# Optimization experiments

Hardware: AMD Instinct MI355X
Metric: run time of the kernel (lower is better)

The kernel has to match this reference:

```python
import jax, jax.numpy as jnp
import numpy as np

B, F, H, OUT, S = 32768, 256, 128, 64, 6
RELAX, EPS, BN_EPS = 1.5, 1e-05, 1e-05
SQRT_HALF = 0.7071067811865476


def _bn(h, g, b):
    # training-mode BatchNorm1d: biased batch statistics over dim 0
    m = h.mean(axis=0)
    v = h.var(axis=0)
    return (h - m) * jax.lax.rsqrt(v + BN_EPS) * g + b


def _tfrm(x, W, g, b, glu_act=True):
    h = _bn(x @ W, g, b)
    if glu_act:
        d = h.shape[1] // 2
        h = h[:, :d] * jax.nn.sigmoid(h[:, d:])
    return h


def setup_inputs() -> dict:
    key = jax.random.key(0)
    ks = jax.random.split(key, 6)
    f32 = jnp.float32
    return {
        "x": jax.random.normal(ks[0], (B, F), f32),
        "enc_g": jnp.ones((F,), f32), "enc_b": jnp.zeros((F,), f32),
        "W1": jax.random.normal(ks[1], (F, 2 * H), f32) * 0.05,
        "g1": jnp.ones((2 * H,), f32), "b1": jnp.zeros((2 * H,), f32),
        "W2": jax.random.normal(ks[2], (H, 2 * H), f32) * 0.05,
        "g2": jnp.ones((2 * H,), f32), "b2": jnp.zeros((2 * H,), f32),
        "W3": jax.random.normal(ks[3], (S, H, 2 * H), f32) * 0.05,
        "g3": jnp.ones((S, 2 * H), f32), "b3": jnp.zeros((S, 2 * H), f32),
        "W4": jax.random.normal(ks[4], (S, H, 2 * H), f32) * 0.05,
        "g4": jnp.ones((S, 2 * H), f32), "b4": jnp.zeros((S, 2 * H), f32),
        "Wc": jax.random.normal(ks[5], (S - 1, OUT, F), f32) * 0.05,
        "gc": jnp.ones((S - 1, F), f32), "bc": jnp.zeros((S - 1, F), f32),
    }


def reference(x, enc_g, enc_b, W1, g1, b1, W2, g2, b2, W3, g3, b3,
              W4, g4, b4, Wc, gc, bc):
    x = _bn(x, enc_g, enc_b)                      # [B, F]
    masked = x
    compl = jnp.ones((x.shape[0], F), x.dtype)    # complementary aggregated mask
    agg_out, agg_entropy = [], []
    for ni in range(S):
        h = _tfrm(masked, W1, g1, b1)                             # [B, H]
        h = (_tfrm(h, W2, g2, b2) + h) * SQRT_HALF
        h = (_tfrm(h, W3[ni], g3[ni], b3[ni]) + h) * SQRT_HALF
        h = (_tfrm(h, W4[ni], g4[ni], b4[ni]) + h) * SQRT_HALF
        if ni > 0:
            # NOTE: source uses x (not h) here -- replicated faithfully
            agg_out.append(jax.nn.relu(x[:, :OUT]))
        fc = h[:, OUT:]                                           # [B, OUT]
        if ni < S - 1:
            coef = _tfrm(fc, Wc[ni], gc[ni], bc[ni], glu_act=False)  # [B, F]
            mask_values = jax.nn.softmax(coef * compl, axis=1)
            compl = compl * (RELAX - mask_values)
            agg_entropy.append(
                jnp.mean(jnp.sum(-mask_values * jnp.log(mask_values + EPS), axis=1))
                / (S - 1))
            masked = mask_values * x
    out = jnp.sum(jnp.stack(agg_out, axis=0), axis=0)   # [B, OUT]
    entropy = jnp.sum(jnp.stack(agg_entropy))           # scalar
    return (out, entropy)
```

## Files before the change

kernel.cpp:

```cpp
#include <hip/hip_runtime.h>
#include <math.h>

#define BSZ   32768
#define FDIM  256
#define HDIM  128
#define OUTD  64
#define SQRT_HALF 0.70710678118654752f
#define BN_EPS 1e-5f
#define SM_EPS 1e-5f
#define INV_B (1.0f / 32768.0f)
#define NCPY  8
#define SLOT  (NCPY * 512)
#define GRID  1024

#define SWZ(r, cb) ((((r) << 9) + (cb)) ^ (((r) & 7) << 4))

typedef __attribute__((ext_vector_type(8))) short bf16x8;
typedef __attribute__((ext_vector_type(4))) short bf16x4;
typedef __attribute__((ext_vector_type(4))) float f32x4;

__device__ __forceinline__ float b2f(unsigned short u) {
    return __uint_as_float(((unsigned int)u) << 16);
}
__device__ __forceinline__ unsigned short f2b(float f) {
    unsigned int u = __float_as_uint(f);
    u += 0x7fff + ((u >> 16) & 1);
    return (unsigned short)(u >> 16);
}

__device__ __forceinline__ void async16(const void* g, void* l) {
    __builtin_amdgcn_global_load_lds(
        (const __attribute__((address_space(1))) void*)(uintptr_t)g,
        (__attribute__((address_space(3))) void*)(unsigned int)(uintptr_t)l,
        16, 0, 0);
}

__device__ inline float waveMaxAll(float v) {
#pragma unroll
    for (int m = 32; m > 0; m >>= 1) v = fmaxf(v, __shfl_xor(v, m, 64));
    return v;
}
__device__ inline float waveSumAll(float v) {
#pragma unroll
    for (int m = 32; m > 0; m >>= 1) v += __shfl_xor(v, m, 64);
    return v;
}

__device__ __forceinline__ void grid_sync_tree(unsigned int* arr, unsigned int want,
                                               int bid, int tid) {
    __syncthreads();
    if (tid == 0) {
        __threadfence();
        __hip_atomic_fetch_add(&arr[(bid & 63) << 5], 1u,
                               __ATOMIC_RELEASE, __HIP_MEMORY_SCOPE_AGENT);
    }
    if (tid < 64) {
        unsigned int* p = &arr[tid << 5];
        long spin = 0;
        while (__hip_atomic_load(p, __ATOMIC_ACQUIRE, __HIP_MEMORY_SCOPE_AGENT) < want) {
            if (++spin > (1L << 24)) break;
            __builtin_amdgcn_s_sleep(1);
        }
        __threadfence();
    }
    __syncthreads();
}

__device__ __forceinline__ void stage_B(short* Bs, const unsigned short* __restrict__ Wt,
                                        int K, int k0, int wave, int lane) {
    const int sr = lane >> 2;
    const int sc = (lane & 3) * 8;
#pragma unroll
    for (int t = 0; t < 4; ++t) {
        const int wr = wave * 64 + t * 16 + sr;
        async16(Wt + (size_t)wr * K + k0 + sc, (void*)(Bs + (wave * 4 + t) * 512 + lane * 8));
    }
}

__device__ __forceinline__ void gemm_core(const short* buf, short* Bs,
                                          const unsigned short* __restrict__ Wt, int K,
                                          int wave, int lane, f32x4 (&acc)[2][4]) {
    const int fm = lane & 15;
    const int fq = (lane >> 4) * 8;
#pragma unroll
    for (int i = 0; i < 2; ++i)
#pragma unroll
        for (int j = 0; j < 4; ++j)
            acc[i][j] = (f32x4){0.f, 0.f, 0.f, 0.f};

    for (int k0 = 0; k0 < K; k0 += 32) {
        __syncthreads();
        bf16x8 af[2], bfr[4];
#pragma unroll
        for (int i = 0; i < 2; ++i)
            af[i] = *(const bf16x8*)((const char*)buf + SWZ(i * 16 + fm, (k0 + fq) * 2));
#pragma unroll
        for (int j = 0; j < 4; ++j)
            bfr[j] = *(const bf16x8*)(Bs + (wave * 64 + j * 16 + fm) * 32 + fq);
#pragma unroll
        for (int i = 0; i < 2; ++i)
#pragma unroll
            for (int j = 0; j < 4; ++j)
                acc[i][j] = __builtin_amdgcn_mfma_f32_16x16x32_bf16(af[i], bfr[j], acc[i][j], 0, 0, 0);
        __syncthreads();
        if (k0 + 32 < K) stage_B(Bs, Wt, K, k0 + 32, wave, lane);
    }
}

__device__ __forceinline__ void stage_epilogue(f32x4 (&acc)[2][4], short* buf,
                                               float* redS, float* redQ,
                                               float* __restrict__ statsOut,
                                               int wave, int lane, int tid, int bcp) {
    const int fm = lane & 15;
    const int row4 = (lane >> 4) * 4;
    const int ocol = wave * 64 + fm;
#pragma unroll
    for (int i = 0; i < 2; ++i)
#pragma unroll
        for (int j = 0; j < 4; ++j)
#pragma unroll
            for (int r = 0; r < 4; ++r)
                *(short*)((char*)buf + SWZ(row4 + i * 16 + r, (ocol + j * 16) * 2)) =
                    (short)f2b(acc[i][j][r]);

#pragma unroll
    for (int j = 0; j < 4; ++j) {
        float s = 0.f, q = 0.f;
#pragma unroll
        for (int i = 0; i < 2; ++i)
#pragma unroll
            for (int r = 0; r < 4; ++r) {
                float v = acc[i][j][r];
                s += v; q += v * v;
            }
        s += __shfl_xor(s, 16, 64); s += __shfl_xor(s, 32, 64);
        q += __shfl_xor(q, 16, 64); q += __shfl_xor(q, 32, 64);
        if (lane < 16) {
            redS[wave * 64 + j * 16 + lane] = s;
            redQ[wave * 64 + j * 16 + lane] = q;
        }
    }
    __syncthreads();
    atomicAdd(&statsOut[bcp + tid], redS[tid]);
    atomicAdd(&statsOut[bcp + 256 + tid], redQ[tid]);
}

__device__ __forceinline__ void build_tbl_glu(const float* __restrict__ st,
                                              const float* __restrict__ pg,
                                              const float* __restrict__ pb,
                                              int colOff, int K, int tid, float* tbl) {
    if (tid < K) {
        const int ch = colOff + tid;
        const int cg = ch + 128;
        float sA = 0.f, qA = 0.f, sG = 0.f, qG = 0.f;
#pragma unroll
        for (int cp = 0; cp < NCPY; ++cp) {
            const float* p = st + cp * 512;
            sA += p[ch]; qA += p[256 + ch];
            sG += p[cg]; qG += p[256 + cg];
        }
        float ma = sA * INV_B, va = qA * INV_B - ma * ma;
        float scA = pg[ch] * rsqrtf(va + BN_EPS);
        tbl[tid] = scA; tbl[K + tid] = pb[ch] - ma * scA;
        float mg = sG * INV_B, vg = qG * INV_B - mg * mg;
        float scG = pg[cg] * rsqrtf(vg + BN_EPS);
        tbl[2 * K + tid] = scG; tbl[3 * K + tid] = pb[cg] - mg * scG;
    }
    __syncthreads();
}

__device__ __forceinline__ void build_tbl_mask(const float* __restrict__ st,
                                               const float* __restrict__ gcp,
                                               const float* __restrict__ bcp_,
                                               int tid, float* tbl) {
    float s = 0.f, q = 0.f;
#pragma unroll
    for (int cp = 0; cp < NCPY; ++cp) {
        s += st[cp * 512 + tid];
        q += st[cp * 512 + 256 + tid];
    }
    float mean = s * INV_B, var = q * INV_B - mean * mean;
    float scl = gcp[tid] * rsqrtf(var + BN_EPS);
    tbl[tid] = scl;
    tbl[256 + tid] = bcp_[tid] - mean * scl;
    __syncthreads();
}

template <int K, bool RES, bool WH, int RB>
__device__ __forceinline__ void glu_prologue(short* buf, const float* tbl,
                                             int tid, int colOff, bf16x4* h) {
    const int ar = tid >> 3;
    const int ac = (tid & 7) * 4;
#pragma unroll
    for (int c = 0; c < K / 32; ++c) {
        const int kk = c * 32 + ac;
        bf16x4 lo = *(const bf16x4*)((const char*)buf + SWZ(ar, (colOff + kk) * 2));
        bf16x4 hi = *(const bf16x4*)((const char*)buf + SWZ(ar, (colOff + kk + 128) * 2));
        float4 a0 = *(const float4*)&tbl[kk];
        float4 h0 = *(const float4*)&tbl[K + kk];
        float4 g0 = *(const float4*)&tbl[2 * K + kk];
        float4 s0 = *(const float4*)&tbl[3 * K + kk];
        const float scA[4] = {a0.x, a0.y, a0.z, a0.w};
        const float shA[4] = {h0.x, h0.y, h0.z, h0.w};
        const float scG[4] = {g0.x, g0.y, g0.z, g0.w};
        const float shG[4] = {s0.x, s0.y, s0.z, s0.w};
        bf16x4 o4;
#pragma unroll
        for (int e = 0; e < 4; ++e) {
            float na = b2f((unsigned short)lo[e]) * scA[e] + shA[e];
            float ng = b2f((unsigned short)hi[e]) * scG[e] + shG[e];
            float v = na * (1.0f / (1.0f + __expf(-ng)));
            if (RES) v = (v + b2f((unsigned short)h[RB + c][e])) * SQRT_HALF;
            o4[e] = (short)f2b(v);
        }
        *(bf16x4*)((char*)buf + SWZ(ar, kk * 2)) = o4;
        if (WH) h[c] = o4;
    }
}

template <int MODE>
__device__ __forceinline__ void mask_phase(short* buf, const float* tbl,
                                           const unsigned short* __restrict__ xb,
                                           unsigned short* cmpl, float* ent, float* went,
                                           int tid, int wave, int lane, int row0, int bid) {
    const int r = tid >> 3;
    const int cq = tid & 7;
    const size_t grow = (size_t)(row0 + r) * 256;

    float l[32];
    float mx = -1e30f;
#pragma unroll
    for (int e = 0; e < 4; ++e) {
        const int c = cq * 32 + e * 8;
        bf16x8 pv = *(const bf16x8*)((const char*)buf + SWZ(r, c * 2));
        bf16x8 cv;
        if (MODE != 0) cv = *(const bf16x8*)(cmpl + grow + c);
        float4 s0 = *(const float4*)&tbl[c], s1 = *(const float4*)&tbl[c + 4];
        float4 h0 = *(const float4*)&tbl[256 + c], h1 = *(const float4*)&tbl[256 + c + 4];
        const float* sp0 = (const float*)&s0; const float* sp1 = (const float*)&s1;
        const float* hp0 = (const float*)&h0; const float* hp1 = (const float*)&h1;
#pragma unroll
        for (int t = 0; t < 8; ++t) {
            float scl = (t < 4) ? sp0[t] : sp1[t - 4];
            float shf = (t < 4) ? hp0[t] : hp1[t - 4];
            float cl = (MODE != 0) ? b2f((unsigned short)cv[t]) : 1.0f;
            float v = (b2f((unsigned short)pv[t]) * scl + shf) * cl;
            l[e * 8 + t] = v;
            mx = fmaxf(mx, v);
        }
    }
    mx = fmaxf(mx, __shfl_xor(mx, 1, 64));
    mx = fmaxf(mx, __shfl_xor(mx, 2, 64));
    mx = fmaxf(mx, __shfl_xor(mx, 4, 64));

    float ssum = 0.f;
#pragma unroll
    for (int i = 0; i < 32; ++i) { l[i] = __expf(l[i] - mx); ssum += l[i]; }
    ssum += __shfl_xor(ssum, 1, 64);
    ssum += __shfl_xor(ssum, 2, 64);
    ssum += __shfl_xor(ssum, 4, 64);
    const float inv = 1.0f / ssum;

    float et = 0.f;
#pragma unroll
    for (int e = 0; e < 4; ++e) {
        const int c = cq * 32 + e * 8;
        bf16x8 xv, cv2;
        if (MODE != 2) xv = *(const bf16x8*)(xb + grow + c);
        if (MODE == 1) cv2 = *(const bf16x8*)(cmpl + grow + c);
        bf16x8 mo, co;
#pragma unroll
        for (int t = 0; t < 8; ++t) {
            float m = l[e * 8 + t] * inv;
            et -= m * __logf(m + SM_EPS);
            if (MODE != 2) {
                float cl = (MODE == 1) ? b2f((unsigned short)cv2[t]) : 1.0f;
                co[t] = (short)f2b(cl * (1.5f - m));
                mo[t] = (short)f2b(m * b2f((unsigned short)xv[t]));
            }
        }
        if (MODE != 2) {
            *(bf16x8*)(cmpl + grow + c) = co;
            *(bf16x8*)((char*)buf + SWZ(r, c * 2)) = mo;
        }
    }
    et += __shfl_xor(et, 1, 64);
    et += __shfl_xor(et, 2, 64);
    et += __shfl_xor(et, 4, 64);
    float wet = waveSumAll(et) * 0.125f;
    if (lane == 0) went[wave] = wet;
    __syncthreads();
    if (tid == 0) {
        float v = went[0] + went[1] + went[2] + went[3];
        atomicAdd(&ent[(bid & 255) << 5], v * (INV_B * 0.2f));
    }
}

__global__ __launch_bounds__(256, 4) void mega(
    const float* __restrict__ x,
    const float* __restrict__ enc_g, const float* __restrict__ enc_b,
    const float* __restrict__ g1, const float* __restrict__ b1,
    const float* __restrict__ g2, const float* __restrict__ b2,
    const float* __restrict__ g3, const float* __restrict__ b3,
    const float* __restrict__ g4, const float* __restrict__ b4,
    const float* __restrict__ gc, const float* __restrict__ bc,
    const float* __restrict__ W1f, const float* __restrict__ W2f,
    const float* __restrict__ W3f, const float* __restrict__ W4f,
    const float* __restrict__ Wcf,
    unsigned short* __restrict__ W1t, unsigned short* __restrict__ W2t,
    unsigned short* __restrict__ W3t, unsigned short* __restrict__ W4t,
    unsigned short* __restrict__ Wct,
    unsigned short* __restrict__ xb, unsigned short* __restrict__ cmpl,
    float* __restrict__ stats, float* __restrict__ ent,
    unsigned int* __restrict__ bar,
    float* __restrict__ out)
{
    __shared__ short buf[32 * 256];
    __shared__ short Bs[256 * 32];
    __shared__ float redS[256], redQ[256];
    __shared__ float tbl[512];
    __shared__ float went[4];

    const int tid  = threadIdx.x;
    const int wave = tid >> 6;
    const int lane = tid & 63;
    const int bid  = blockIdx.x;
    const int row0 = bid * 32;
    const int bcp  = (bid & (NCPY - 1)) * 512;

    unsigned int bgen = 0;
#define GSYNC() do { ++bgen; grid_sync_tree(bar, bgen * 16u, bid, tid); } while (0)

    if (bid < 136) {
        const int m = bid >> 3, kz = bid & 7, n = tid;
        const float* src; unsigned short* dst; int K;
        if (m == 0)      { src = W1f;                        dst = W1t;               K = 256; }
        else if (m == 1) { src = W2f;                        dst = W2t;               K = 128; }
        else if (m < 7)  { int i = m - 2;  src = W3f + (size_t)i * 128 * 256; dst = W3t + (size_t)i * 32768; K = 128; }
        else if (m < 12) { int i = m - 7;  src = W4f + (size_t)i * 128 * 256; dst = W4t + (size_t)i * 32768; K = 128; }
        else             { int i = m - 12; src = Wcf + (size_t)i * 64 * 256;  dst = Wct + (size_t)i * 16384; K = 64; }
        const int k0 = kz * 32;
        if (k0 < K)
            for (int k = k0; k < k0 + 32; ++k)
                dst[(size_t)n * K + k] = f2b(src[(size_t)k * 256 + n]);
    }
    {
        float* red = (float*)buf;
        const int sub = wave;
        const int c4  = lane << 2;
        float s[4] = {0.f, 0.f, 0.f, 0.f}, q[4] = {0.f, 0.f, 0.f, 0.f};
#pragma unroll 8
        for (int i = 0; i < 8; ++i) {
            const int row = row0 + i * 4 + sub;
            float4 v = *(const float4*)(x + (size_t)row * 256 + c4);
            s[0] += v.x; q[0] += v.x * v.x;
            s[1] += v.y; q[1] += v.y * v.y;
            s[2] += v.z; q[2] += v.z * v.z;
            s[3] += v.w; q[3] += v.w * v.w;
        }
#pragma unroll
        for (int e = 0; e < 4; ++e) {
            red[sub * 512 + c4 + e] = s[e];
            red[sub * 512 + 256 + c4 + e] = q[e];
        }
        __syncthreads();
        float sS = red[tid] + red[512 + tid] + red[1024 + tid] + red[1536 + tid];
        float sQ = red[256 + tid] + red[768 + tid] + red[1280 + tid] + red[1792 + tid];
        atomicAdd(&stats[bcp + tid], sS);
        atomicAdd(&stats[bcp + 256 + tid], sQ);
    }
    GSYNC();

    stage_B(Bs, W1t, 256, 0, wave, lane);
    {
        float s = 0.f, q = 0.f;
#pragma unroll
        for (int cp = 0; cp < NCPY; ++cp) {
            s += stats[cp * 512 + tid];
            q += stats[cp * 512 + 256 + tid];
        }
        float mean = s * INV_B, var = q * INV_B - mean * mean;
        float scl = enc_g[tid] * rsqrtf(var + BN_EPS);
        tbl[tid] = scl;
        tbl[256 + tid] = enc_b[tid] - mean * scl;
    }
    __syncthreads();
    {
        const int r = tid >> 3, cq = tid & 7;
        const size_t grow = (size_t)(row0 + r) * 256;
#pragma unroll
        for (int e = 0; e < 4; ++e) {
            const int c = cq * 32 + e * 8;
            float4 xa = *(const float4*)(x + grow + c);
            float4 xc = *(const float4*)(x + grow + c + 4);
            const float xv[8] = {xa.x, xa.y, xa.z, xa.w, xc.x, xc.y, xc.z, xc.w};
            float4 s0 = *(const float4*)&tbl[c], s1 = *(const float4*)&tbl[c + 4];
            float4 f0 = *(const float4*)&tbl[256 + c], f1 = *(const float4*)&tbl[256 + c + 4];
            const float sc[8] = {s0.x, s0.y, s0.z, s0.w, s1.x, s1.y, s1.z, s1.w};
            const float sh[8] = {f0.x, f0.y, f0.z, f0.w, f1.x, f1.y, f1.z, f1.w};
            float n[8];
            bf16x8 o8;
#pragma unroll
            for (int t = 0; t < 8; ++t) {
                n[t] = xv[t] * sc[t] + sh[t];
                o8[t] = (short)f2b(n[t]);
            }
            *(bf16x8*)((char*)buf + SWZ(r, c * 2)) = o8;
            *(bf16x8*)(xb + grow + c) = o8;
            if (c < OUTD) {
                float4 o1 = make_float4(5.f * fmaxf(n[0], 0.f), 5.f * fmaxf(n[1], 0.f),
                                        5.f * fmaxf(n[2], 0.f), 5.f * fmaxf(n[3], 0.f));
                float4 o2 = make_float4(5.f * fmaxf(n[4], 0.f), 5.f * fmaxf(n[5], 0.f),
                                        5.f * fmaxf(n[6], 0.f), 5.f * fmaxf(n[7], 0.f));
                *(float4*)(out + (size_t)(row0 + r) * OUTD + c) = o1;
                *(float4*)(out + (size_t)(row0 + r) * OUTD + c + 4) = o2;
            }
        }
    }

    f32x4 acc[2][4];
    bf16x4 h[4];

    for (int ni = 0; ni < 5; ++ni) {
        float* s1 = stats + (size_t)(1 + ni * 5 + 0) * SLOT;
        float* s2 = stats + (size_t)(1 + ni * 5 + 1) * SLOT;
        float* s3 = stats + (size_t)(1 + ni * 5 + 2) * SLOT;
        float* s4 = stats + (size_t)(1 + ni * 5 + 3) * SLOT;
        float* s5 = stats + (size_t)(1 + ni * 5 + 4) * SLOT;

        if (ni > 0) {
            float* s5p = stats + (size_t)(1 + (ni - 1) * 5 + 4) * SLOT;
            build_tbl_mask(s5p, gc + (ni - 1) * 256, bc + (ni - 1) * 256, tid, tbl);
            if (ni == 1)
                mask_phase<0>(buf, tbl, xb, cmpl, ent, went, tid, wave, lane, row0, bid);
            else
                mask_phase<1>(buf, tbl, xb, cmpl, ent, went, tid, wave, lane, row0, bid);
        }
        gemm_core(buf, Bs, W1t, 256, wave, lane, acc);
        stage_epilogue(acc, buf, redS, redQ, s1, wave, lane, tid, bcp);
        stage_B(Bs, W2t, 128, 0, wave, lane);
        GSYNC();

        build_tbl_glu(s1, g1, b1, 0, 128, tid, tbl);
        glu_prologue<128, false, true, 0>(buf, tbl, tid, 0, h);
        gemm_core(buf, Bs, W2t, 128, wave, lane, acc);
        stage_epilogue(acc, buf, redS, redQ, s2, wave, lane, tid, bcp);
        stage_B(Bs, W3t + (size_t)ni * 32768, 128, 0, wave, lane);
        GSYNC();

        build_tbl_glu(s2, g2, b2, 0, 128, tid, tbl);
        glu_prologue<128, true, true, 0>(buf, tbl, tid, 0, h);
        gemm_core(buf, Bs, W3t + (size_t)ni * 32768, 128, wave, lane, acc);
        stage_epilogue(acc, buf, redS, redQ, s3, wave, lane, tid, bcp);
        stage_B(Bs, W4t + (size_t)ni * 32768, 128, 0, wave, lane);
        GSYNC();

        build_tbl_glu(s3, g3 + ni * 256, b3 + ni * 256, 0, 128, tid, tbl);
        glu_prologue<128, true, true, 0>(buf, tbl, tid, 0, h);
        gemm_core(buf, Bs, W4t + (size_t)ni * 32768, 128, wave, lane, acc);
        stage_epilogue(acc, buf, redS, redQ, s4, wave, lane, tid, bcp);
        stage_B(Bs, Wct + (size_t)ni * 16384, 64, 0, wave, lane);
        GSYNC();

        build_tbl_glu(s4, g4 + ni * 256, b4 + ni * 256, 64, 64, tid, tbl);
        glu_prologue<64, true, false, 2>(buf, tbl, tid, 64, h);
        gemm_core(buf, Bs, Wct + (size_t)ni * 16384, 64, wave, lane, acc);
        stage_epilogue(acc, buf, redS, redQ, s5, wave, lane, tid, bcp);
        if (ni < 4) stage_B(Bs, W1t, 256, 0, wave, lane);
        GSYNC();
    }

    build_tbl_mask(stats + (size_t)(1 + 4 * 5 + 4) * SLOT,
                   gc + 4 * 256, bc + 4 * 256, tid, tbl);
    mask_phase<2>(buf, tbl, xb, cmpl, ent, went, tid, wave, lane, row0, bid);
    GSYNC();

    if (bid == 0 && wave == 0) {
        float v = 0.f;
#pragma unroll
        for (int i = 0; i < 4; ++i) v += ent[(lane + 64 * i) << 5];
        v = waveSumAll(v);
        if (lane == 0) out[(size_t)BSZ * OUTD] = v;
    }
#undef GSYNC
}

__global__ __launch_bounds__(256) void prep_w(
    const float* __restrict__ W1, const float* __restrict__ W2,
    const float* __restrict__ W3, const float* __restrict__ W4,
    const float* __restrict__ Wc,
    unsigned short* __restrict__ W1t, unsigned short* __restrict__ W2t,
    unsigned short* __restrict__ W3t, unsigned short* __restrict__ W4t,
    unsigned short* __restrict__ Wct)
{
    const int m = blockIdx.x, kz = blockIdx.y, n = threadIdx.x;
    const float* src; unsigned short* dst; int K;
    if (m == 0)      { src = W1;                        dst = W1t;               K = 256; }
    else if (m == 1) { src = W2;                        dst = W2t;               K = 128; }
    else if (m < 7)  { int i = m - 2;  src = W3 + (size_t)i * 128 * 256; dst = W3t + (size_t)i * 32768; K = 128; }
    else if (m < 12) { int i = m - 7;  src = W4 + (size_t)i * 128 * 256; dst = W4t + (size_t)i * 32768; K = 128; }
    else             { int i = m - 12; src = Wc + (size_t)i * 64 * 256;  dst = Wct + (size_t)i * 16384; K = 64; }
    const int k0 = kz * 32;
    if (k0 >= K) return;
    for (int k = k0; k < k0 + 32; ++k)
        dst[(size_t)n * K + k] = f2b(src[(size_t)k * 256 + n]);
}

__global__ __launch_bounds__(256) void colstats(const float* __restrict__ X,
                                                float* __restrict__ st0) {
    __shared__ float red[4][512];
    const int sub = threadIdx.x >> 6;
    const int c4  = (threadIdx.x & 63) << 2;
    float s[4] = {0.f, 0.f, 0.f, 0.f}, q[4] = {0.f, 0.f, 0.f, 0.f};
#pragma unroll 8
    for (int i = 0; i < 8; ++i) {
        const int row = blockIdx.x * 32 + i * 4 + sub;
        float4 v = *(const float4*)(X + (size_t)row * 256 + c4);
        s[0] += v.x; q[0] += v.x * v.x;
        s[1] += v.y; q[1] += v.y * v.y;
        s[2] += v.z; q[2] += v.z * v.z;
        s[3] += v.w; q[3] += v.w * v.w;
    }
#pragma unroll
    for (int e = 0; e < 4; ++e) {
        red[sub][c4 + e] = s[e];
        red[sub][256 + c4 + e] = q[e];
    }
    __syncthreads();
    const int t = threadIdx.x;
    const int cp = (blockIdx.x & (NCPY - 1)) * 512;
    float sS = red[0][t] + red[1][t] + red[2][t] + red[3][t];
    float sQ = red[0][256 + t] + red[1][256 + t] + red[2][256 + t] + red[3][256 + t];
    atomicAdd(&st0[cp + t], sS);
    atomicAdd(&st0[cp + 256 + t], sQ);
}

__global__ __launch_bounds__(256) void norm_x(const float* __restrict__ x,
                                              const float* __restrict__ st0,
                                              const float* __restrict__ g,
                                              const float* __restrict__ b,
                                              unsigned short* __restrict__ xb,
                                              float* __restrict__ out) {
    const int i4 = blockIdx.x * 256 + threadIdx.x;
    const int row = i4 >> 6, c4 = (i4 & 63) << 2;
    float4 xv = *(const float4*)(x + (size_t)row * 256 + c4);
    float sS[4] = {0.f, 0.f, 0.f, 0.f}, sQ[4] = {0.f, 0.f, 0.f, 0.f};
#pragma unroll
    for (int cp = 0; cp < NCPY; ++cp) {
        float4 a = *(const float4*)&st0[cp * 512 + c4];
        float4 q = *(const float4*)&st0[cp * 512 + 256 + c4];
        sS[0] += a.x; sS[1] += a.y; sS[2] += a.z; sS[3] += a.w;
        sQ[0] += q.x; sQ[1] += q.y; sQ[2] += q.z; sQ[3] += q.w;
    }
    float4 gv = *(const float4*)&g[c4];
    float4 bv = *(const float4*)&b[c4];
    const float* xp = (const float*)&xv;
    const float* gp = (const float*)&gv; const float* bp = (const float*)&bv;
    float n[4];
    ushort4 ob;
    unsigned short* obp = (unsigned short*)&ob;
#pragma unroll
    for (int e = 0; e < 4; ++e) {
        float mean = sS[e] * INV_B;
        float var  = sQ[e] * INV_B - mean * mean;
        float sc   = gp[e] * rsqrtf(var + BN_EPS);
        float sh   = bp[e] - mean * sc;
        n[e] = xp[e] * sc + sh;
        obp[e] = f2b(n[e]);
    }
    *(ushort4*)(xb + (size_t)row * 256 + c4) = ob;
    if (c4 < OUTD) {
        float4 ov = make_float4(5.0f * fmaxf(n[0], 0.f), 5.0f * fmaxf(n[1], 0.f),
                                5.0f * fmaxf(n[2], 0.f), 5.0f * fmaxf(n[3], 0.f));
        *(float4*)(out + (size_t)row * OUTD + c4) = ov;
    }
}

__device__ __forceinline__ void gemm_epilogue(
    f32x4 (&acc)[2][4], int row0, int wave, int lane, int tid, int bcp,
    float* redS, float* redQ,
    unsigned short* __restrict__ Pout, float* __restrict__ statsOut)
{
    const int fm = lane & 15;
    const int orow = row0 + (lane >> 4) * 4;
    const int ocol = wave * 64 + fm;
#pragma unroll
    for (int i = 0; i < 2; ++i)
#pragma unroll
        for (int j = 0; j < 4; ++j)
#pragma unroll
            for (int r = 0; r < 4; ++r)
                Pout[(size_t)(orow + i * 16 + r) * 256 + (ocol + j * 16)] = f2b(acc[i][j][r]);

#pragma unroll
    for (int j = 0; j < 4; ++j) {
        float s = 0.f, q = 0.f;
#pragma unroll
        for (int i = 0; i < 2; ++i)
#pragma unroll
            for (int r = 0; r < 4; ++r) {
                float v = acc[i][j][r];
                s += v; q += v * v;
            }
        s += __shfl_xor(s, 16, 64); s += __shfl_xor(s, 32, 64);
        q += __shfl_xor(q, 16, 64); q += __shfl_xor(q, 32, 64);
        if (lane < 16) {
            redS[wave * 64 + j * 16 + lane] = s;
            redQ[wave * 64 + j * 16 + lane] = q;
        }
    }
    __syncthreads();
    atomicAdd(&statsOut[bcp + tid], redS[tid]);
    atomicAdd(&statsOut[bcp + 256 + tid], redQ[tid]);
}

__global__ __launch_bounds__(256) void gemm_bf16(
    const unsigned short* __restrict__ A,
    const unsigned short* __restrict__ Wt, int K,
    unsigned short* __restrict__ P,
    float* __restrict__ statsOut)
{
    __shared__ short As[32 * 32];
    __shared__ short Bs[256 * 32];
    __shared__ float redS[256], redQ[256];

    const int tid  = threadIdx.x;
    const int wave = tid >> 6;
    const int lane = tid & 63;
    const int row0 = blockIdx.x * 32;
    const int bcp  = (blockIdx.x & (NCPY - 1)) * 512;

    const int sr = lane >> 2;
    const int sc = (lane & 3) * 8;
    const int fm = lane & 15;
    const int fq = (lane >> 4) * 8;

    f32x4 acc[2][4];
#pragma unroll
    for (int i = 0; i < 2; ++i)
#pragma unroll
        for (int j = 0; j < 4; ++j)
            acc[i][j] = (f32x4){0.f, 0.f, 0.f, 0.f};

    for (int k0 = 0; k0 < K; k0 += 32) {
        if (wave < 2)
            async16(A + (size_t)(row0 + wave * 16 + sr) * K + k0 + sc,
                    (void*)(As + wave * 512 + lane * 8));
#pragma unroll
        for (int t = 0; t < 4; ++t) {
            const int wr = wave * 64 + t * 16 + sr;
            async16(Wt + (size_t)wr * K + k0 + sc,
                    (void*)(Bs + (wave * 4 + t) * 512 + lane * 8));
        }
        __syncthreads();

        bf16x8 af[2], bfr[4];
#pragma unroll
        for (int i = 0; i < 2; ++i)
            af[i] = *(const bf16x8*)(As + (i * 16 + fm) * 32 + fq);
#pragma unroll
        for (int j = 0; j < 4; ++j)
            bfr[j] = *(const bf16x8*)(Bs + (wave * 64 + j * 16 + fm) * 32 + fq);
#pragma unroll
        for (int i = 0; i < 2; ++i)
#pragma unroll
            for (int j = 0; j < 4; ++j)
                acc[i][j] = __builtin_amdgcn_mfma_f32_16x16x32_bf16(af[i], bfr[j], acc[i][j], 0, 0, 0);
        __syncthreads();
    }

    gemm_epilogue(acc, row0, wave, lane, tid, bcp, redS, redQ, P, statsOut);
}

template <int MODE>
__global__ __launch_bounds__(256) void gemm_mask(
    const unsigned short* Pc,
    const float* __restrict__ cstats,
    const float* __restrict__ gc, const float* __restrict__ bc,
    const unsigned short* __restrict__ xb,
    unsigned short* __restrict__ cmpl,
    float* __restrict__ ent,
    const unsigned short* __restrict__ Wt,
    unsigned short* Pout,
    float* __restrict__ statsOut)
{
    __shared__ short Am[32 * 256];
    __shared__ short Bs[256 * 32];
    __shared__ float redS[256], redQ[256];
    __shared__ float tScl[256], tShf[256];
    __shared__ float went[4];

    const int tid  = threadIdx.x;
    const int wave = tid >> 6;
    const int lane = tid & 63;
    const int row0 = blockIdx.x * 32;
    const int bcp  = (blockIdx.x & (NCPY - 1)) * 512;

    const int sr = lane >> 2;
    const int sc = (lane & 3) * 8;

#pragma unroll
    for (int t = 0; t < 4; ++t) {
        const int wr = wave * 64 + t * 16 + sr;
        async16(Wt + (size_t)wr * 256 + sc,
                (void*)(Bs + (wave * 4 + t) * 512 + lane * 8));
    }

    {
        float s = 0.f, q = 0.f;
#pragma unroll
        for (int cp = 0; cp < NCPY; ++cp) {
            s += cstats[cp * 512 + tid];
            q += cstats[cp * 512 + 256 + tid];
        }
        float mean = s * INV_B, var = q * INV_B - mean * mean;
        float scl_ = gc[tid] * rsqrtf(var + BN_EPS);
        tScl[tid] = scl_;
        tShf[tid] = bc[tid] - mean * scl_;
    }
    __syncthreads();

    const int r  = tid >> 3;
    const int cq = tid & 7;
    const size_t grow = (size_t)(row0 + r) * 256;

    float l[32];
    float mx = -1e30f;
#pragma unroll
    for (int e = 0; e < 4; ++e) {
        const int c = cq * 32 + e * 8;
        bf16x8 pv = *(const bf16x8*)(Pc + grow + c);
        bf16x8 cv;
        if (MODE) cv = *(const bf16x8*)(cmpl + grow + c);
        float4 s0 = *(const float4*)&tScl[c], s1 = *(const float4*)&tScl[c + 4];
        float4 h0 = *(const float4*)&tShf[c], h1 = *(const float4*)&tShf[c + 4];
        const float* sp0 = (const float*)&s0; const float* sp1 = (const float*)&s1;
        const float* hp0 = (const float*)&h0; const float* hp1 = (const float*)&h1;
#pragma unroll
        for (int t = 0; t < 8; ++t) {
            float scl_ = (t < 4) ? sp0[t] : sp1[t - 4];
            float shf_ = (t < 4) ? hp0[t] : hp1[t - 4];
            float cl = MODE ? b2f((unsigned short)cv[t]) : 1.0f;
            float v = (b2f((unsigned short)pv[t]) * scl_ + shf_) * cl;
            l[e * 8 + t] = v;
            mx = fmaxf(mx, v);
        }
    }
    mx = fmaxf(mx, __shfl_xor(mx, 1, 64));
    mx = fmaxf(mx, __shfl_xor(mx, 2, 64));
    mx = fmaxf(mx, __shfl_xor(mx, 4, 64));

    float ssum = 0.f;
#pragma unroll
    for (int i = 0; i < 32; ++i) { l[i] = __expf(l[i] - mx); ssum += l[i]; }
    ssum += __shfl_xor(ssum, 1, 64);
    ssum += __shfl_xor(ssum, 2, 64);
    ssum += __shfl_xor(ssum, 4, 64);
    const float inv = 1.0f / ssum;

    float et = 0.f;
#pragma unroll
    for (int e = 0; e < 4; ++e) {
        const int c = cq * 32 + e * 8;
        bf16x8 xv = *(const bf16x8*)(xb + grow + c);
        bf16x8 cv2;
        if (MODE) cv2 = *(const bf16x8*)(cmpl + grow + c);
        bf16x8 mo, co;
#pragma unroll
        for (int t = 0; t < 8; ++t) {
            float m = l[e * 8 + t] * inv;
            et -= m * __logf(m + SM_EPS);
            float cl = MODE ? b2f((unsigned short)cv2[t]) : 1.0f;
            co[t] = (short)f2b(cl * (1.5f - m));
            mo[t] = (short)f2b(m * b2f((unsigned short)xv[t]));
        }
        *(bf16x8*)(cmpl + grow + c) = co;
        unsigned int byte = (unsigned int)(r * 512 + c * 2);
        byte ^= ((unsigned int)(r & 7)) << 4;
        *(bf16x8*)((char*)Am + byte) = mo;
    }
    et += __shfl_xor(et, 1, 64);
    et += __shfl_xor(et, 2, 64);
    et += __shfl_xor(et, 4, 64);
    float wet = waveSumAll(et) * 0.125f;
    if (lane == 0) went[wave] = wet;
    __syncthreads();
    if (tid == 0) {
        float v = went[0] + went[1] + went[2] + went[3];
        atomicAdd(&ent[(blockIdx.x & 255) << 5], v * (INV_B * 0.2f));
    }

    const int fm = lane & 15;
    const int fq = (lane >> 4) * 8;

    f32x4 acc[2][4];
#pragma unroll
    for (int i = 0; i < 2; ++i)
#pragma unroll
        for (int j = 0; j < 4; ++j)
            acc[i][j] = (f32x4){0.f, 0.f, 0.f, 0.f};

    for (int k0 = 0; k0 < 256; k0 += 32) {
        bf16x8 af[2], bfr[4];
#pragma unroll
        for (int i = 0; i < 2; ++i) {
            const int row = i * 16 + fm;
            unsigned int byte = (unsigned int)(row * 512 + (k0 + fq) * 2);
            byte ^= ((unsigned int)(row & 7)) << 4;
            af[i] = *(const bf16x8*)((const char*)Am + byte);
        }
#pragma unroll
        for (int j = 0; j < 4; ++j)
            bfr[j] = *(const bf16x8*)(Bs + (wave * 64 + j * 16 + fm) * 32 + fq);
#pragma unroll
        for (int i = 0; i < 2; ++i)
#pragma unroll
            for (int j = 0; j < 4; ++j)
                acc[i][j] = __builtin_amdgcn_mfma_f32_16x16x32_bf16(af[i], bfr[j], acc[i][j], 0, 0, 0);
        __syncthreads();
        if (k0 + 32 < 256) {
#pragma unroll
            for (int t = 0; t < 4; ++t) {
                const int wr = wave * 64 + t * 16 + sr;
                async16(Wt + (size_t)wr * 256 + (k0 + 32) + sc,
                        (void*)(Bs + (wave * 4 + t) * 512 + lane * 8));
            }
            __syncthreads();
        }
    }

    gemm_epilogue(acc, row0, wave, lane, tid, bcp, redS, redQ, Pout, statsOut);
}

template <bool RES, bool WRITE_H>
__global__ __launch_bounds__(256) void gemm_glu(
    const unsigned short* __restrict__ Pprev,
    const float* __restrict__ pstats,
    const float* __restrict__ pg,
    const float* __restrict__ pb,
    const unsigned short* __restrict__ res,
    int colOff,
    const unsigned short* __restrict__ Wt, int K,
    unsigned short* __restrict__ Pout,
    float* __restrict__ statsOut,
    unsigned short* __restrict__ hOut)
{
    __shared__ short As[32 * 32];
    __shared__ short Bs[256 * 32];
    __shared__ float redS[256], redQ[256];
    __shared__ float tScA[128], tShA[128], tScG[128], tShG[128];

    const int tid  = threadIdx.x;
    const int wave = tid >> 6;
    const int lane = tid & 63;
    const int row0 = blockIdx.x * 32;
    const int bcp  = (blockIdx.x & (NCPY - 1)) * 512;

    if (tid < K) {
        const int ch = colOff + tid;
        const int cg = ch + 128;
        float sA = 0.f, qA = 0.f, sG = 0.f, qG = 0.f;
#pragma unroll
        for (int cp = 0; cp < NCPY; ++cp) {
            const float* p = pstats + cp * 512;
            sA += p[ch]; qA += p[256 + ch];
            sG += p[cg]; qG += p[256 + cg];
        }
        float ma = sA * INV_B, va = qA * INV_B - ma * ma;
        float scA = pg[ch] * rsqrtf(va + BN_EPS);
        tScA[tid] = scA; tShA[tid] = pb[ch] - ma * scA;
        float mg = sG * INV_B, vg = qG * INV_B - mg * mg;
        float scG = pg[cg] * rsqrtf(vg + BN_EPS);
        tScG[tid] = scG; tShG[tid] = pb[cg] - mg * scG;
    }
    __syncthreads();

    const int sr = lane >> 2;
    const int sc = (lane & 3) * 8;
    const int ar = tid >> 3;
    const int ac = (tid & 7) * 4;
    const int fm = lane & 15;
    const int fq = (lane >> 4) * 8;

    f32x4 acc[2][4];
#pragma unroll
    for (int i = 0; i < 2; ++i)
#pragma unroll
        for (int j = 0; j < 4; ++j)
            acc[i][j] = (f32x4){0.f, 0.f, 0.f, 0.f};

    for (int k0 = 0; k0 < K; k0 += 32) {
#pragma unroll
        for (int t = 0; t < 4; ++t) {
            const int wr = wave * 64 + t * 16 + sr;
            async16(Wt + (size_t)wr * K + k0 + sc,
                    (void*)(Bs + (wave * 4 + t) * 512 + lane * 8));
        }

        {
            const int kk = k0 + ac;
            const size_t grow = (size_t)(row0 + ar);

            bf16x4 lo = *(const bf16x4*)(Pprev + grow * 256 + colOff + kk);
            bf16x4 hi = *(const bf16x4*)(Pprev + grow * 256 + colOff + kk + 128);
            bf16x4 rv;
            if (RES) rv = *(const bf16x4*)(res + grow * 128 + kk);

            float4 a0 = *(const float4*)&tScA[kk];
            float4 h0 = *(const float4*)&tShA[kk];
            float4 g0 = *(const float4*)&tScG[kk];
            float4 s0 = *(const float4*)&tShG[kk];
            float scA[4] = {a0.x, a0.y, a0.z, a0.w};
            float shA[4] = {h0.x, h0.y, h0.z, h0.w};
            float scG[4] = {g0.x, g0.y, g0.z, g0.w};
            float shG[4] = {s0.x, s0.y, s0.z, s0.w};

            bf16x4 o4;
#pragma unroll
            for (int e = 0; e < 4; ++e) {
                float na = b2f((unsigned short)lo[e]) * scA[e] + shA[e];
                float ng = b2f((unsigned short)hi[e]) * scG[e] + shG[e];
                float v = na * (1.0f / (1.0f + __expf(-ng)));
                if (RES) v = (v + b2f((unsigned short)rv[e])) * SQRT_HALF;
                o4[e] = (short)f2b(v);
            }
            *(bf16x4*)(As + ar * 32 + ac) = o4;
            if (WRITE_H)
                *(bf16x4*)(hOut + grow * 128 + kk) = o4;
        }
        __syncthreads();

        bf16x8 af[2], bfr[4];
#pragma unroll
        for (int i = 0; i < 2; ++i)
            af[i] = *(const bf16x8*)(As + (i * 16 + fm) * 32 + fq);
#pragma unroll
        for (int j = 0; j < 4; ++j)
            bfr[j] = *(const bf16x8*)(Bs + (wave * 64 + j * 16 + fm) * 32 + fq);
#pragma unroll
        for (int i = 0; i < 2; ++i)
#pragma unroll
            for (int j = 0; j < 4; ++j)
                acc[i][j] = __builtin_amdgcn_mfma_f32_16x16x32_bf16(af[i], bfr[j], acc[i][j], 0, 0, 0);
        __syncthreads();
    }

    gemm_epilogue(acc, row0, wave, lane, tid, bcp, redS, redQ, Pout, statsOut);
}

__global__ __launch_bounds__(256) void coef_ent(const unsigned short* __restrict__ Pc,
                                                const float* __restrict__ stats,
                                                const float* __restrict__ gc,
                                                const float* __restrict__ bc,
                                                const unsigned short* __restrict__ cmpl,
                                                float* __restrict__ ent) {
    const int w    = threadIdx.x >> 6;
    const int lane = threadIdx.x & 63;
    const int row  = blockIdx.x * 4 + w;
    const int c    = lane << 2;
    __shared__ float went[4];

    float sS[4] = {0.f, 0.f, 0.f, 0.f}, sQ[4] = {0.f, 0.f, 0.f, 0.f};
#pragma unroll
    for (int cp = 0; cp < NCPY; ++cp) {
        float4 a = *(const float4*)&stats[cp * 512 + c];
        float4 q = *(const float4*)&stats[cp * 512 + 256 + c];
        sS[0] += a.x; sS[1] += a.y; sS[2] += a.z; sS[3] += a.w;
        sQ[0] += q.x; sQ[1] += q.y; sQ[2] += q.z; sQ[3] += q.w;
    }
    float4 gv = *(const float4*)&gc[c];
    float4 bv = *(const float4*)&bc[c];
    const float* gvv = (const float*)&gv; const float* bvv = (const float*)&bv;

    float scl[4], shf[4];
#pragma unroll
    for (int e = 0; e < 4; ++e) {
        float mean = sS[e] * INV_B, var = sQ[e] * INV_B - mean * mean;
        scl[e] = gvv[e] * rsqrtf(var + BN_EPS);
        shf[e] = bvv[e] - mean * scl[e];
    }

    const size_t idx = (size_t)row * 256 + c;
    ushort4 pu = *(const ushort4*)(Pc + idx);
    const unsigned short* puv = (const unsigned short*)&pu;
    ushort4 cu = *(const ushort4*)(cmpl + idx);
    const unsigned short* cuv = (const unsigned short*)&cu;

    float l[4];
#pragma unroll
    for (int e = 0; e < 4; ++e)
        l[e] = (b2f(puv[e]) * scl[e] + shf[e]) * b2f(cuv[e]);

    float mx = waveMaxAll(fmaxf(fmaxf(l[0], l[1]), fmaxf(l[2], l[3])));
    float e0 = __expf(l[0] - mx), e1 = __expf(l[1] - mx),
          e2 = __expf(l[2] - mx), e3 = __expf(l[3] - mx);
    float inv = 1.0f / waveSumAll(e0 + e1 + e2 + e3);

    float m[4] = {e0 * inv, e1 * inv, e2 * inv, e3 * inv};

    float et = -m[0] * __logf(m[0] + SM_EPS) - m[1] * __logf(m[1] + SM_EPS)
             - m[2] * __logf(m[2] + SM_EPS) - m[3] * __logf(m[3] + SM_EPS);
    et = waveSumAll(et);
    if (lane == 0) went[w] = et;
    __syncthreads();
    if (threadIdx.x == 0) {
        float v = went[0] + went[1] + went[2] + went[3];
        atomicAdd(&ent[(blockIdx.x & 255) << 5], v * (INV_B * 0.2f));
    }
}

__global__ __launch_bounds__(64) void write_ent(const float* __restrict__ ent,
                                                float* __restrict__ dst) {
    const int lane = threadIdx.x;
    float v = 0.f;
#pragma unroll
    for (int i = 0; i < 4; ++i) v += ent[(lane + 64 * i) << 5];
    v = waveSumAll(v);
    if (lane == 0) dst[0] = v;
}

extern "C" void kernel_launch(void* const* d_in, const int* in_sizes, int n_in,
                              void* d_out, int out_size, void* d_ws, size_t ws_size,
                              hipStream_t stream) {
    const float* x     = (const float*)d_in[0];
    const float* enc_g = (const float*)d_in[1];
    const float* enc_b = (const float*)d_in[2];
    const float* W1 = (const float*)d_in[3];
    const float* g1 = (const float*)d_in[4];
    const float* b1 = (const float*)d_in[5];
    const float* W2 = (const float*)d_in[6];
    const float* g2 = (const float*)d_in[7];
    const float* b2 = (const float*)d_in[8];
    const float* W3 = (const float*)d_in[9];
    const float* g3 = (const float*)d_in[10];
    const float* b3 = (const float*)d_in[11];
    const float* W4 = (const float*)d_in[12];
    const float* g4 = (const float*)d_in[13];
    const float* b4 = (const float*)d_in[14];
    const float* Wc = (const float*)d_in[15];
    const float* gc = (const float*)d_in[16];
    const float* bc = (const float*)d_in[17];
    float* out = (float*)d_out;

    const size_t NBF = (size_t)BSZ * FDIM;
    const size_t NBH = (size_t)BSZ * HDIM;

    unsigned short* xb     = (unsigned short*)d_ws;
    unsigned short* masked = xb + NBF;
    unsigned short* Pb1    = masked + NBF;
    unsigned short* h1     = Pb1 + NBF;
    unsigned short* h2     = h1 + NBH;
    unsigned short* h3     = h2 + NBH;
    unsigned short* cmpl   = h3 + NBH;
    unsigned short* W1t    = cmpl + NBF;
    unsigned short* W2t    = W1t + 65536;
    unsigned short* W3t    = W2t + 32768;
    unsigned short* W4t    = W3t + 163840;
    unsigned short* Wct    = W4t + 163840;
    float* stats = (float*)(Wct + 81920);
    float* ent   = stats + 26 * SLOT;
    unsigned int* bar = (unsigned int*)masked;

    unsigned short* Pb2 = masked;

    static int s_ok = -1;
    if (s_ok < 0) {
        int occ = 0, mpc = 0, dev = 0;
        hipGetDevice(&dev);
        hipDeviceProp_t prop;
        if (hipGetDeviceProperties(&prop, dev) == hipSuccess) mpc = prop.multiProcessorCount;
        if (hipOccupancyMaxActiveBlocksPerMultiprocessor(
                &occ, reinterpret_cast<const void*>(mega), 256, 0) != hipSuccess) occ = 0;
        s_ok = (occ >= 4 && occ * mpc >= GRID) ? 1 : 0;
    }

    hipMemsetAsync(stats, 0, (26 * SLOT + 256 * 32) * sizeof(float), stream);

    if (s_ok) {
        hipMemsetAsync(bar, 0, 64 * 32 * sizeof(unsigned int), stream);
        mega<<<GRID, 256, 0, stream>>>(
            x, enc_g, enc_b, g1, b1, g2, b2, g3, b3, g4, b4, gc, bc,
            W1, W2, W3, W4, Wc, W1t, W2t, W3t, W4t, Wct,
            xb, cmpl, stats, ent, bar, out);
        return;
    }

    prep_w<<<dim3(17, 8), 256, 0, stream>>>(W1, W2, W3, W4, Wc, W1t, W2t, W3t, W4t, Wct);
    colstats<<<1024, 256, 0, stream>>>(x, stats);
    norm_x<<<8192, 256, 0, stream>>>(x, stats, enc_g, enc_b, xb, out);

    for (int ni = 0; ni < 5; ++ni) {
        float* s1 = stats + (size_t)(1 + ni * 5 + 0) * SLOT;
        float* s2 = stats + (size_t)(1 + ni * 5 + 1) * SLOT;
        float* s3 = stats + (size_t)(1 + ni * 5 + 2) * SLOT;
        float* s4 = stats + (size_t)(1 + ni * 5 + 3) * SLOT;
        float* s5 = stats + (size_t)(1 + ni * 5 + 4) * SLOT;

        if (ni == 0) {
            gemm_bf16<<<1024, 256, 0, stream>>>(xb, W1t, 256, Pb1, s1);
        } else {
            float* s5p = stats + (size_t)(1 + (ni - 1) * 5 + 4) * SLOT;
            if (ni == 1)
                gemm_mask<0><<<1024, 256, 0, stream>>>(
                    Pb1, s5p, gc, bc, xb, cmpl, ent, W1t, Pb1, s1);
            else
                gemm_mask<1><<<1024, 256, 0, stream>>>(
                    Pb1, s5p, gc + (ni - 1) * 256, bc + (ni - 1) * 256,
                    xb, cmpl, ent, W1t, Pb1, s1);
        }

        gemm_glu<false, true><<<1024, 256, 0, stream>>>(
            Pb1, s1, g1, b1, nullptr, 0, W2t, 128, Pb2, s2, h1);
        gemm_glu<true, true><<<1024, 256, 0, stream>>>(
            Pb2, s2, g2, b2, h1, 0, W3t + (size_t)ni * 32768, 128, Pb1, s3, h2);
        gemm_glu<true, true><<<1024, 256, 0, stream>>>(
            Pb1, s3, g3 + ni * 256, b3 + ni * 256, h2, 0,
            W4t + (size_t)ni * 32768, 128, Pb2, s4, h3);
        gemm_glu<true, false><<<1024, 256, 0, stream>>>(
            Pb2, s4, g4 + ni * 256, b4 + ni * 256, h3 + 64, 64,
            Wct + (size_t)ni * 16384, 64, Pb1, s5, nullptr);
    }

    coef_ent<<<BSZ / 4, 256, 0, stream>>>(
        Pb1, stats + (size_t)(1 + 4 * 5 + 4) * SLOT,
        gc + 4 * 256, bc + 4 * 256, cmpl, ent);

    write_ent<<<1, 64, 0, stream>>>(ent, out + (size_t)BSZ * OUTD);
}
```

Before: 560.2 us.

## Use leader-release grid barrier and drop per-k block barriers in GEMM

The grid barrier changes from every block polling all 64 counters to a scheme where block 0 polls the counters and then publishes a release flag. All other blocks spin on that one flag with a single thread. The GEMM k-loop replaces its two __syncthreads per iteration with explicit s_waitcnt instructions and a sched_barrier, keeping one block barrier before and after the loop. Both changes aim to cut synchronisation overhead in a persistent megakernel. The GEMM change risks races: each wave's B tile is loaded by that same wave, but the A operand sits in a shared buffer and there is no block barrier between iterations.

```diff
diff --git a/kernel.cpp b/kernel.cpp
--- a/kernel.cpp
+++ b/kernel.cpp
@@ -46,22 +46,36 @@
     return v;
 }
 
-__device__ __forceinline__ void grid_sync_tree(unsigned int* arr, unsigned int want,
-                                               int bid, int tid) {
+__device__ __forceinline__ void grid_sync_lr(unsigned int* arr, unsigned int* rel,
+                                             unsigned int gen, int bid, int tid) {
     __syncthreads();
     if (tid == 0) {
         __threadfence();
         __hip_atomic_fetch_add(&arr[(bid & 63) << 5], 1u,
                                __ATOMIC_RELEASE, __HIP_MEMORY_SCOPE_AGENT);
     }
-    if (tid < 64) {
-        unsigned int* p = &arr[tid << 5];
-        long spin = 0;
-        while (__hip_atomic_load(p, __ATOMIC_ACQUIRE, __HIP_MEMORY_SCOPE_AGENT) < want) {
-            if (++spin > (1L << 24)) break;
-            __builtin_amdgcn_s_sleep(1);
-        }
-        __threadfence();
+    if (bid == 0) {
+        if (tid < 64) {
+            unsigned int* p = &arr[tid << 5];
+            long spin = 0;
+            while (__hip_atomic_load(p, __ATOMIC_ACQUIRE, __HIP_MEMORY_SCOPE_AGENT) < gen * 16u) {
+                if (++spin > (1L << 24)) break;
+                __builtin_amdgcn_s_sleep(1);
+            }
+            __threadfence();
+        }
+        __syncthreads();
+        if (tid == 0)
+            __hip_atomic_store(rel, gen, __ATOMIC_RELEASE, __HIP_MEMORY_SCOPE_AGENT);
+    } else {
+        if (tid == 0) {
+            long spin = 0;
+            while (__hip_atomic_load(rel, __ATOMIC_ACQUIRE, __HIP_MEMORY_SCOPE_AGENT) < gen) {
+                if (++spin > (1L << 24)) break;
+                __builtin_amdgcn_s_sleep(2);
+            }
+            __threadfence();
+        }
     }
     __syncthreads();
 }
@@ -88,8 +102,10 @@
         for (int j = 0; j < 4; ++j)
             acc[i][j] = (f32x4){0.f, 0.f, 0.f, 0.f};
 
+    __syncthreads();
+
     for (int k0 = 0; k0 < K; k0 += 32) {
-        __syncthreads();
+        asm volatile("s_waitcnt vmcnt(0)" ::: "memory");
         bf16x8 af[2], bfr[4];
 #pragma unroll
         for (int i = 0; i < 2; ++i)
@@ -102,9 +118,13 @@
 #pragma unroll
             for (int j = 0; j < 4; ++j)
                 acc[i][j] = __builtin_amdgcn_mfma_f32_16x16x32_bf16(af[i], bfr[j], acc[i][j], 0, 0, 0);
-        __syncthreads();
-        if (k0 + 32 < K) stage_B(Bs, Wt, K, k0 + 32, wave, lane);
-    }
+        if (k0 + 32 < K) {
+            asm volatile("s_waitcnt lgkmcnt(0)" ::: "memory");
+            __builtin_amdgcn_sched_barrier(0);
+            stage_B(Bs, Wt, K, k0 + 32, wave, lane);
+        }
+    }
+    __syncthreads();
 }
 
 __device__ __forceinline__ void stage_epilogue(f32x4 (&acc)[2][4], short* buf,
@@ -328,8 +348,9 @@
     const int row0 = bid * 32;
     const int bcp  = (bid & (NCPY - 1)) * 512;
 
+    unsigned int* rel = bar + 64 * 32;
     unsigned int bgen = 0;
-#define GSYNC() do { ++bgen; grid_sync_tree(bar, bgen * 16u, bid, tid); } while (0)
+#define GSYNC() do { ++bgen; grid_sync_lr(bar, rel, bgen, bid, tid); } while (0)
 
     if (bid < 136) {
         const int m = bid >> 3, kz = bid & 7, n = tid;
@@ -1077,7 +1098,7 @@
     hipMemsetAsync(stats, 0, (26 * SLOT + 256 * 32) * sizeof(float), stream);
 
     if (s_ok) {
-        hipMemsetAsync(bar, 0, 64 * 32 * sizeof(unsigned int), stream);
+        hipMemsetAsync(bar, 0, 65 * 32 * sizeof(unsigned int), stream);
         mega<<<GRID, 256, 0, stream>>>(
             x, enc_g, enc_b, g1, b1, g2, b2, g3, b3, g4, b4, gc, bc,
             W1, W2, W3, W4, Wc, W1t, W2t, W3t, W4t, Wct,
```

Result: no change. 556.9 us (-0.6%).
